# Optimization experiments

Hardware: AMD Instinct MI355X
Metric: run time of the kernel (lower is better)

## Reference

```python
import jax, jax.numpy as jnp
import numpy as np
from jax.scipy.linalg import solve_triangular

# Production config from MFAWrapper.from_path: 28x28 images, 50 components, 6 factors
B, DFT, K, L = 2048, 784, 50, 6
LOG2PI = float(np.log(2.0 * np.pi))


def setup_inputs() -> dict:
    key = jax.random.key(0)
    k1, k2, k3, k4, k5, k6 = jax.random.split(key, 6)
    X = jax.random.normal(k1, (B, DFT), dtype=jnp.float32)
    J = jax.random.randint(k2, (B, DFT), 0, 2).astype(jnp.int32)  # binary observation mask
    MU = jax.random.normal(k3, (K, DFT), dtype=jnp.float32) * 0.5
    A_fac = jax.random.normal(k4, (K, DFT, L), dtype=jnp.float32) * 0.1  # factor loadings
    log_D = jax.random.normal(k5, (K, DFT), dtype=jnp.float32) * 0.1 - 1.0  # log noise variances
    PI_logits = jax.random.normal(k6, (K,), dtype=jnp.float32)
    return {"X": X, "J": J, "MU": MU, "A_fac": A_fac, "log_D": log_D, "PI_logits": PI_logits}


def _mfa_conditional(X, J, MU, A_fac, log_D, PI_logits):
    """Batched MFA conditional reconstruction given observed features (mask J==1).

    The per-sample torch.nonzero selection is replaced by mask-weighted linear
    algebra: restricting to observed rows of diag(1/D) is identical to zeroing
    the unobserved entries of the weight, so all B samples are conditioned in
    one batched pass instead of a Python loop.
    """
    dtype = X.dtype
    l = A_fac.shape[-1]
    Jf = (J == 1).astype(dtype)                 # [B, Dft]
    inv_D = jnp.exp(-log_D)                     # [K, Dft]
    # masked residual per (sample, component): [B, K, Dft]
    md = (X[:, None, :] - MU[None, :, :]) * Jf[:, None, :]
    # latent posterior precision P = I + A_o^T D_o^{-1} A_o  -> [B, K, L, L]
    P = jnp.einsum('bd,kd,kdi,kdj->bkij', Jf, inv_D, A_fac, A_fac) + jnp.eye(l, dtype=dtype)
    # q = A_o^T D_o^{-1} (x_o - mu_o)  -> [B, K, L]
    q = jnp.einsum('bkd,kd,kdi->bki', md, inv_D, A_fac)
    # per-component log-likelihood of observed features via Woodbury / matrix det lemma
    Lc = jnp.linalg.cholesky(P)                                         # [B, K, L, L]
    y = solve_triangular(Lc, q[..., None], lower=True)[..., 0]          # [B, K, L]
    quad = jnp.einsum('bkd,kd->bk', md * md, inv_D) - jnp.sum(y * y, axis=-1)
    logdet = (2.0 * jnp.sum(jnp.log(jnp.diagonal(Lc, axis1=-2, axis2=-1)), axis=-1)
              + jnp.einsum('bd,kd->bk', Jf, log_D))
    n_obs = jnp.sum(Jf, axis=-1, keepdims=True)                         # [B, 1]
    log_lik = -0.5 * (quad + logdet + n_obs * LOG2PI)                   # [B, K]
    log_resp = jax.nn.log_softmax(PI_logits)[None, :] + log_lik
    c = jnp.argmax(log_resp, axis=-1)                                   # most responsible component, [B]
    # gather per-sample selected component and form the conditional Gaussian in factor form
    P_sel = jnp.take_along_axis(P, c[:, None, None, None], axis=1)[:, 0]  # [B, L, L]
    q_sel = jnp.take_along_axis(q, c[:, None, None], axis=1)[:, 0]        # [B, L]
    A_sel = A_fac[c]                                                      # [B, Dft, L]
    m_z = jnp.linalg.solve(P_sel, q_sel[..., None])[..., 0]               # posterior latent mean [B, L]
    cov_z = jnp.linalg.inv(P_sel)                                         # posterior latent cov [B, L, L]
    Lz = jnp.linalg.cholesky(cov_z)
    M = MU[c] + jnp.einsum('bdi,bi->bd', A_sel, m_z)                      # conditional mean over all features
    A_out = jnp.einsum('bdi,bij->bdj', A_sel, Lz)                         # loadings: cond cov = A_out A_out^T + diag(D_out)
    D_out = jnp.exp(log_D)[c]                                             # [B, Dft]
    Pw = jnp.ones((X.shape[0], 1), dtype)
    return Pw, M, A_out, D_out


def reference(X, J, MU, A_fac, log_D, PI_logits):
    return _mfa_conditional(X, J, MU, A_fac, log_D, PI_logits)
```

## Files before the change

kernel.cpp:

```cpp
#include <hip/hip_runtime.h>
#include <math.h>

#define B_N 2048
#define D_FT 784
#define K_N 50
#define L_N 6
#define LOG2PI_F 1.8378770664093453f

#define OUT_PW 0
#define OUT_M  (B_N)
#define OUT_A  (OUT_M + B_N*D_FT)
#define OUT_D  (OUT_A + B_N*D_FT*6)

#define WS_SCORES 0
#define WS_PQ     (WS_SCORES + K_N*B_N)
#define WS_XT     (WS_PQ + K_N*27*B_N)
#define WS_JBT    (WS_XT + D_FT*B_N)

#define IDX(i,j) ((i)*((i)+1)/2 + (j))

typedef float v2f __attribute__((ext_vector_type(2)));

#define PK_FMA(acc, a, b) asm("v_pk_fma_f32 %0, %1, %2, %0" : "+v"(acc) : "v"(a), "v"(b))
#define PK_MUL(dst, a, b) asm("v_pk_mul_f32 %0, %1, %2" : "=v"(dst) : "v"(a), "v"(b))
#define PK_ADD(dst, a, b) asm("v_pk_add_f32 %0, %1, %2" : "=v"(dst) : "v"(a), "v"(b))

__device__ __forceinline__ void chol6(const float* P, float* L, float* rd, float* sumlog) {
    float sl = 0.f;
    #pragma unroll
    for (int j = 0; j < 6; ++j) {
        float s = P[IDX(j,j)];
        #pragma unroll
        for (int m = 0; m < j; ++m) s -= L[IDX(j,m)] * L[IDX(j,m)];
        float d = sqrtf(s);
        L[IDX(j,j)] = d;
        float r = 1.0f / d;
        rd[j] = r;
        sl += logf(d);
        #pragma unroll
        for (int i = j + 1; i < 6; ++i) {
            float t = P[IDX(i,j)];
            #pragma unroll
            for (int m = 0; m < j; ++m) t -= L[IDX(i,m)] * L[IDX(j,m)];
            L[IDX(i,j)] = t * r;
        }
    }
    *sumlog = sl;
}

__global__ __launch_bounds__(1024) void k_prep(const float* __restrict__ X,
                                               const int* __restrict__ J,
                                               float4* __restrict__ Xt4,
                                               unsigned* __restrict__ JbT) {
    const int bid = blockIdx.x;
    const int tid = threadIdx.x;
    if (bid < 448) {
        __shared__ float4 tile[32][33];
        int tx = tid & 31, ty = tid >> 5;
        int d4b = (bid % 7) * 32;
        int bb  = (bid / 7) * 32;
        int d4 = d4b + tx;
        if (d4 < D_FT / 4)
            tile[ty][tx] = *(const float4*)&X[(size_t)(bb + ty) * D_FT + d4 * 4];
        __syncthreads();
        int d4o = d4b + ty;
        if (d4o < D_FT / 4)
            Xt4[(size_t)d4o * B_N + (bb + tx)] = tile[tx][ty];
    } else {
        int t = (bid - 448) * 1024 + tid;
        int b = t >> 5;
        int w = t & 31;
        if (w >= 25) return;
        int d0 = w * 32;
        int n = D_FT - d0; if (n > 32) n = 32;
        unsigned u = 0;
        for (int j = 0; j < n; ++j)
            u |= (J[(size_t)b * D_FT + d0 + j] != 0 ? 1u : 0u) << j;
        JbT[(size_t)w * B_N + b] = u;
    }
}

#define ACC_PAIR(pi, dd, x0, x1) do { \
    const v2f a0 = sld[(size_t)(pi) * 10 + 0]; \
    const v2f a1 = sld[(size_t)(pi) * 10 + 1]; \
    const v2f a2 = sld[(size_t)(pi) * 10 + 2]; \
    const v2f a3 = sld[(size_t)(pi) * 10 + 3]; \
    const v2f a4 = sld[(size_t)(pi) * 10 + 4]; \
    const v2f a5 = sld[(size_t)(pi) * 10 + 5]; \
    const v2f sa2  = sld[(size_t)(pi) * 10 + 6]; \
    const v2f nmu2 = sld[(size_t)(pi) * 10 + 7]; \
    const v2f l2   = sld[(size_t)(pi) * 10 + 8]; \
    v2f m2; m2.x = (float)((mw >> (dd)) & 1u); m2.y = (float)((mw >> ((dd)+1)) & 1u); \
    v2f x2; x2.x = (x0); x2.y = (x1); \
    v2f xm2; PK_ADD(xm2, x2, nmu2); \
    v2f w2;  PK_MUL(w2, m2, sa2); \
    v2f z2;  PK_MUL(z2, w2, xm2); \
    v2f u0, u1, u2v, u3, u4, u5; \
    PK_MUL(u0, m2, a0); PK_MUL(u1, m2, a1); PK_MUL(u2v, m2, a2); \
    PK_MUL(u3, m2, a3); PK_MUL(u4, m2, a4); PK_MUL(u5, m2, a5); \
    PK_FMA(jld2, m2, l2); \
    PK_FMA(Pm2[0],  u0, a0); \
    PK_FMA(Pm2[1],  u1, a0); PK_FMA(Pm2[2],  u1, a1); \
    PK_FMA(Pm2[3],  u2v, a0); PK_FMA(Pm2[4],  u2v, a1); PK_FMA(Pm2[5],  u2v, a2); \
    PK_FMA(Pm2[6],  u3, a0); PK_FMA(Pm2[7],  u3, a1); PK_FMA(Pm2[8],  u3, a2); PK_FMA(Pm2[9],  u3, a3); \
    PK_FMA(Pm2[10], u4, a0); PK_FMA(Pm2[11], u4, a1); PK_FMA(Pm2[12], u4, a2); PK_FMA(Pm2[13], u4, a3); PK_FMA(Pm2[14], u4, a4); \
    PK_FMA(Pm2[15], u5, a0); PK_FMA(Pm2[16], u5, a1); PK_FMA(Pm2[17], u5, a2); PK_FMA(Pm2[18], u5, a3); PK_FMA(Pm2[19], u5, a4); PK_FMA(Pm2[20], u5, a5); \
    PK_FMA(qv2[0], z2, a0); PK_FMA(qv2[1], z2, a1); PK_FMA(qv2[2], z2, a2); \
    PK_FMA(qv2[3], z2, a3); PK_FMA(qv2[4], z2, a4); PK_FMA(qv2[5], z2, a5); \
    PK_FMA(quad2, z2, z2); \
} while (0)

__global__ __launch_bounds__(256, 3) void k_accum(
        const float4* __restrict__ Xt4, const unsigned* __restrict__ JbT,
        const float* __restrict__ A, const float* __restrict__ MU,
        const float* __restrict__ logD, const float* __restrict__ PI,
        float* __restrict__ scores, float* __restrict__ Pq) {
    __shared__ v2f sld[200 * 10];
    float* smem = (float*)sld;
    float4* smf4 = (float4*)sld;
    const int k   = blockIdx.x >> 5;
    const int tid = threadIdx.x;
    const int s   = tid & 63;
    const int h   = tid >> 6;
    const int b   = (blockIdx.x & 31) * 64 + s;

    v2f Pm2[21], qv2[6], quad2, jld2;
    #pragma unroll
    for (int t = 0; t < 21; ++t) { Pm2[t].x = 0.f; Pm2[t].y = 0.f; }
    #pragma unroll
    for (int t = 0; t < 6; ++t) { qv2[t].x = 0.f; qv2[t].y = 0.f; }
    quad2.x = 0.f; quad2.y = 0.f;
    jld2.x = 0.f; jld2.y = 0.f;
    int nob = 0;

    for (int c = 0; c < 2; ++c) {
        const int dbase = c ? 384 : 0;
        const int npair = c ? 200 : 192;
        __syncthreads();
        for (int p = tid; p < npair; p += 256) {
            const int d0 = dbase + 2 * p;
            const float* ar0 = A + ((size_t)k * D_FT + d0) * 6;
            const float* ar1 = ar0 + 6;
            float ld0 = logD[(size_t)k * D_FT + d0];
            float ld1 = logD[(size_t)k * D_FT + d0 + 1];
            float sa0 = expf(-0.5f * ld0);
            float sa1 = expf(-0.5f * ld1);
            float4 f0, f1, f2, f3, f4;
            f0.x = sa0 * ar0[0]; f0.y = sa1 * ar1[0]; f0.z = sa0 * ar0[1]; f0.w = sa1 * ar1[1];
            f1.x = sa0 * ar0[2]; f1.y = sa1 * ar1[2]; f1.z = sa0 * ar0[3]; f1.w = sa1 * ar1[3];
            f2.x = sa0 * ar0[4]; f2.y = sa1 * ar1[4]; f2.z = sa0 * ar0[5]; f2.w = sa1 * ar1[5];
            f3.x = sa0; f3.y = sa1;
            f3.z = -MU[(size_t)k * D_FT + d0];
            f3.w = -MU[(size_t)k * D_FT + d0 + 1];
            f4.x = ld0; f4.y = ld1; f4.z = 0.f; f4.w = 0.f;
            smf4[(size_t)p * 5 + 0] = f0;
            smf4[(size_t)p * 5 + 1] = f1;
            smf4[(size_t)p * 5 + 2] = f2;
            smf4[(size_t)p * 5 + 3] = f3;
            smf4[(size_t)p * 5 + 4] = f4;
        }
        __syncthreads();

        const int wb = (c ? 12 : 0) + 3 * h;
        for (int w = wb; w < wb + 3; ++w) {
            const unsigned mw = JbT[(size_t)w * B_N + b];
            nob += __popc(mw);
            const int plb = w * 16 - (dbase >> 1);
            const float4* xp = Xt4 + (size_t)(w * 8) * B_N + b;
            #pragma unroll 2
            for (int g = 0; g < 8; ++g) {
                float4 xv = xp[(size_t)g * B_N];
                ACC_PAIR(plb + 2 * g,     g * 4,     xv.x, xv.y);
                ACC_PAIR(plb + 2 * g + 1, g * 4 + 2, xv.z, xv.w);
            }
        }
        if (c == 1 && h == 3) {
            const unsigned mw = JbT[(size_t)24 * B_N + b];
            nob += __popc(mw);
            const int plb = 24 * 16 - 192;
            const float4* xp = Xt4 + (size_t)(24 * 8) * B_N + b;
            #pragma unroll
            for (int g = 0; g < 4; ++g) {
                float4 xv = xp[(size_t)g * B_N];
                ACC_PAIR(plb + 2 * g,     g * 4,     xv.x, xv.y);
                ACC_PAIR(plb + 2 * g + 1, g * 4 + 2, xv.z, xv.w);
            }
        }
    }

    float Pm[21], qv[6], quad, jld;
    #pragma unroll
    for (int t = 0; t < 21; ++t) Pm[t] = Pm2[t].x + Pm2[t].y;
    #pragma unroll
    for (int t = 0; t < 6; ++t) qv[t] = qv2[t].x + qv2[t].y;
    quad = quad2.x + quad2.y;
    jld  = jld2.x + jld2.y;

    __syncthreads();
    float* red = smem;
    #define SLAB_WR do { float* o = &red[s * 33]; \
        _Pragma("unroll") for (int t = 0; t < 21; ++t) o[t] = Pm[t]; \
        _Pragma("unroll") for (int t = 0; t < 6; ++t) o[21 + t] = qv[t]; \
        o[27] = quad; o[28] = (float)nob; o[29] = jld; } while (0)
    #define SLAB_ADD do { const float* o = &red[s * 33]; \
        _Pragma("unroll") for (int t = 0; t < 21; ++t) Pm[t] += o[t]; \
        _Pragma("unroll") for (int t = 0; t < 6; ++t) qv[t] += o[21 + t]; \
        quad += o[27]; nob += (int)o[28]; jld += o[29]; } while (0)

    if (h == 1) SLAB_WR;
    __syncthreads();
    if (h == 0) SLAB_ADD;
    __syncthreads();
    if (h == 3) SLAB_WR;
    __syncthreads();
    if (h == 2) SLAB_ADD;
    __syncthreads();
    if (h == 2) SLAB_WR;
    __syncthreads();
    if (h == 0) {
        SLAB_ADD;
        float nobs = (float)nob;

        Pm[0] += 1.f; Pm[2] += 1.f; Pm[5] += 1.f; Pm[9] += 1.f; Pm[14] += 1.f; Pm[20] += 1.f;

        float Lm[21], rd[6], sumlog;
        chol6(Pm, Lm, rd, &sumlog);
        float y[6];
        #pragma unroll
        for (int j = 0; j < 6; ++j) {
            float sv = qv[j];
            #pragma unroll
            for (int m = 0; m < j; ++m) sv -= Lm[IDX(j,m)] * y[m];
            y[j] = sv * rd[j];
        }
        float yy = 0.f;
        #pragma unroll
        for (int j = 0; j < 6; ++j) yy += y[j] * y[j];
        float logdet = 2.f * sumlog + jld;
        float ll = -0.5f * ((quad - yy) + logdet + nobs * LOG2PI_F);
        float score = ll + PI[k];

        scores[(size_t)k * B_N + b] = score;
        float* pq = Pq + (size_t)k * 27 * B_N + b;
        #pragma unroll
        for (int t = 0; t < 21; ++t) pq[(size_t)t * B_N] = Pm[t];
        #pragma unroll
        for (int t = 0; t < 6; ++t) pq[(size_t)(21 + t) * B_N] = qv[t];
    }
}

__global__ __launch_bounds__(256) void k_outsel(
        const float* __restrict__ scores, const float* __restrict__ Pq,
        const float* __restrict__ A, const float* __restrict__ MU,
        const float* __restrict__ logD, float* __restrict__ out) {
    __shared__ float smz[6];
    __shared__ float sLz[21];
    __shared__ int sc;
    const int b = blockIdx.x;
    const int tid = threadIdx.x;

    if (tid < 64) {
        float best = scores[b];
        int bc = 0;
        for (int kk = 1; kk < K_N; ++kk) {
            float sv = scores[(size_t)kk * B_N + b];
            if (sv > best) { best = sv; bc = kk; }
        }

        float Pm[21], qv[6];
        const float* pq = Pq + (size_t)bc * 27 * B_N + b;
        #pragma unroll
        for (int t = 0; t < 21; ++t) Pm[t] = pq[(size_t)t * B_N];
        #pragma unroll
        for (int t = 0; t < 6; ++t) qv[t] = pq[(size_t)(21 + t) * B_N];

        float Lm[21], rd[6], dummy;
        chol6(Pm, Lm, rd, &dummy);

        float y[6];
        #pragma unroll
        for (int j = 0; j < 6; ++j) {
            float sv = qv[j];
            #pragma unroll
            for (int m = 0; m < j; ++m) sv -= Lm[IDX(j,m)] * y[m];
            y[j] = sv * rd[j];
        }
        float mz[6];
        #pragma unroll
        for (int ii = 5; ii >= 0; --ii) {
            float sv = y[ii];
            #pragma unroll
            for (int j = ii + 1; j < 6; ++j) sv -= Lm[IDX(j,ii)] * mz[j];
            mz[ii] = sv * rd[ii];
        }
        float Li[21];
        #pragma unroll
        for (int j = 0; j < 6; ++j) {
            Li[IDX(j,j)] = rd[j];
            #pragma unroll
            for (int i = j + 1; i < 6; ++i) {
                float sv = 0.f;
                #pragma unroll
                for (int m = j; m < i; ++m) sv += Lm[IDX(i,m)] * Li[IDX(m,j)];
                Li[IDX(i,j)] = -sv * rd[i];
            }
        }
        float cov[21];
        #pragma unroll
        for (int i = 0; i < 6; ++i) {
            #pragma unroll
            for (int j = 0; j <= i; ++j) {
                float sv = 0.f;
                #pragma unroll
                for (int m = i; m < 6; ++m) sv += Li[IDX(m,i)] * Li[IDX(m,j)];
                cov[IDX(i,j)] = sv;
            }
        }
        float Lz[21], rd2[6];
        chol6(cov, Lz, rd2, &dummy);

        if (tid == 0) {
            sc = bc;
            out[OUT_PW + b] = 1.0f;
            #pragma unroll
            for (int t = 0; t < 6; ++t) smz[t] = mz[t];
            #pragma unroll
            for (int t = 0; t < 21; ++t) sLz[t] = Lz[t];
        }
    }
    __syncthreads();
    const int c = sc;

    for (int d = tid; d < D_FT; d += 256) {
        const float* ar = A + ((size_t)c * D_FT + d) * 6;
        float a[6];
        #pragma unroll
        for (int i = 0; i < 6; ++i) a[i] = ar[i];
        float mu = MU[(size_t)c * D_FT + d];
        float ld = logD[(size_t)c * D_FT + d];
        float m = mu;
        #pragma unroll
        for (int i = 0; i < 6; ++i) m += a[i] * smz[i];
        out[OUT_M + (size_t)b * D_FT + d] = m;
        out[OUT_D + (size_t)b * D_FT + d] = expf(ld);
        float* ao = out + OUT_A + ((size_t)b * D_FT + d) * 6;
        #pragma unroll
        for (int j = 0; j < 6; ++j) {
            float sv = 0.f;
            #pragma unroll
            for (int i = j; i < 6; ++i) sv += a[i] * sLz[IDX(i,j)];
            ao[j] = sv;
        }
    }
}

extern "C" void kernel_launch(void* const* d_in, const int* in_sizes, int n_in,
                              void* d_out, int out_size, void* d_ws, size_t ws_size,
                              hipStream_t stream) {
    (void)in_sizes; (void)n_in; (void)out_size; (void)ws_size;
    const float* X    = (const float*)d_in[0];
    const int*   J    = (const int*)d_in[1];
    const float* MU   = (const float*)d_in[2];
    const float* A    = (const float*)d_in[3];
    const float* logD = (const float*)d_in[4];
    const float* PI   = (const float*)d_in[5];
    float* out = (float*)d_out;
    float* ws  = (float*)d_ws;

    float*    scores = ws + WS_SCORES;
    float*    Pq     = ws + WS_PQ;
    float4*   Xt4    = (float4*)(ws + WS_XT);
    unsigned* JbT    = (unsigned*)(ws + WS_JBT);

    k_prep<<<512, 1024, 0, stream>>>(X, J, Xt4, JbT);

    k_accum<<<32 * K_N, 256, 0, stream>>>(Xt4, JbT, A, MU, logD, PI, scores, Pq);

    k_outsel<<<B_N, 256, 0, stream>>>(scores, Pq, A, MU, logD, out);
}
```

Before: 116.1 us.

## Precompute per-component weight records and read them via scalar constant loads

Adds a prep stage that writes per-component records holding A, exp(-logD) and -MU, plus a separate logD array, to the workspace. The accumulation kernel no longer stages these into LDS with block barriers. It reads them through address_space(4) pointers so the compiler can issue wave-uniform scalar loads, and the packed v_pk_fma math becomes scalar fmaf. This removes the LDS fill and its syncs and lowers LDS use, but drops the packed-FP32 throughput and needs an extra workspace region.

```diff
diff --git a/kernel.cpp b/kernel.cpp
--- a/kernel.cpp
+++ b/kernel.cpp
@@ -16,14 +16,12 @@
 #define WS_PQ     (WS_SCORES + K_N*B_N)
 #define WS_XT     (WS_PQ + K_N*27*B_N)
 #define WS_JBT    (WS_XT + D_FT*B_N)
+#define WS_WREC   (WS_JBT + 25*B_N)
+#define WS_WLD    (WS_WREC + K_N*D_FT*8)
 
 #define IDX(i,j) ((i)*((i)+1)/2 + (j))
 
-typedef float v2f __attribute__((ext_vector_type(2)));
-
-#define PK_FMA(acc, a, b) asm("v_pk_fma_f32 %0, %1, %2, %0" : "+v"(acc) : "v"(a), "v"(b))
-#define PK_MUL(dst, a, b) asm("v_pk_mul_f32 %0, %1, %2" : "=v"(dst) : "v"(a), "v"(b))
-#define PK_ADD(dst, a, b) asm("v_pk_add_f32 %0, %1, %2" : "=v"(dst) : "v"(a), "v"(b))
+#define CAS const __attribute__((address_space(4)))
 
 __device__ __forceinline__ void chol6(const float* P, float* L, float* rd, float* sumlog) {
     float sl = 0.f;
@@ -50,8 +48,13 @@
 
 __global__ __launch_bounds__(1024) void k_prep(const float* __restrict__ X,
                                                const int* __restrict__ J,
+                                               const float* __restrict__ A,
+                                               const float* __restrict__ MU,
+                                               const float* __restrict__ logD,
                                                float4* __restrict__ Xt4,
-                                               unsigned* __restrict__ JbT) {
+                                               unsigned* __restrict__ JbT,
+                                               float* __restrict__ Wrec,
+                                               float* __restrict__ Wld) {
     const int bid = blockIdx.x;
     const int tid = threadIdx.x;
     if (bid < 448) {
@@ -66,7 +69,7 @@
         int d4o = d4b + ty;
         if (d4o < D_FT / 4)
             Xt4[(size_t)d4o * B_N + (bb + tx)] = tile[tx][ty];
-    } else {
+    } else if (bid < 512) {
         int t = (bid - 448) * 1024 + tid;
         int b = t >> 5;
         int w = t & 31;
@@ -77,127 +80,101 @@
         for (int j = 0; j < n; ++j)
             u |= (J[(size_t)b * D_FT + d0 + j] != 0 ? 1u : 0u) << j;
         JbT[(size_t)w * B_N + b] = u;
-    }
-}
-
-#define ACC_PAIR(pi, dd, x0, x1) do { \
-    const v2f a0 = sld[(size_t)(pi) * 10 + 0]; \
-    const v2f a1 = sld[(size_t)(pi) * 10 + 1]; \
-    const v2f a2 = sld[(size_t)(pi) * 10 + 2]; \
-    const v2f a3 = sld[(size_t)(pi) * 10 + 3]; \
-    const v2f a4 = sld[(size_t)(pi) * 10 + 4]; \
-    const v2f a5 = sld[(size_t)(pi) * 10 + 5]; \
-    const v2f sa2  = sld[(size_t)(pi) * 10 + 6]; \
-    const v2f nmu2 = sld[(size_t)(pi) * 10 + 7]; \
-    const v2f l2   = sld[(size_t)(pi) * 10 + 8]; \
-    v2f m2; m2.x = (float)((mw >> (dd)) & 1u); m2.y = (float)((mw >> ((dd)+1)) & 1u); \
-    v2f x2; x2.x = (x0); x2.y = (x1); \
-    v2f xm2; PK_ADD(xm2, x2, nmu2); \
-    v2f w2;  PK_MUL(w2, m2, sa2); \
-    v2f z2;  PK_MUL(z2, w2, xm2); \
-    v2f u0, u1, u2v, u3, u4, u5; \
-    PK_MUL(u0, m2, a0); PK_MUL(u1, m2, a1); PK_MUL(u2v, m2, a2); \
-    PK_MUL(u3, m2, a3); PK_MUL(u4, m2, a4); PK_MUL(u5, m2, a5); \
-    PK_FMA(jld2, m2, l2); \
-    PK_FMA(Pm2[0],  u0, a0); \
-    PK_FMA(Pm2[1],  u1, a0); PK_FMA(Pm2[2],  u1, a1); \
-    PK_FMA(Pm2[3],  u2v, a0); PK_FMA(Pm2[4],  u2v, a1); PK_FMA(Pm2[5],  u2v, a2); \
-    PK_FMA(Pm2[6],  u3, a0); PK_FMA(Pm2[7],  u3, a1); PK_FMA(Pm2[8],  u3, a2); PK_FMA(Pm2[9],  u3, a3); \
-    PK_FMA(Pm2[10], u4, a0); PK_FMA(Pm2[11], u4, a1); PK_FMA(Pm2[12], u4, a2); PK_FMA(Pm2[13], u4, a3); PK_FMA(Pm2[14], u4, a4); \
-    PK_FMA(Pm2[15], u5, a0); PK_FMA(Pm2[16], u5, a1); PK_FMA(Pm2[17], u5, a2); PK_FMA(Pm2[18], u5, a3); PK_FMA(Pm2[19], u5, a4); PK_FMA(Pm2[20], u5, a5); \
-    PK_FMA(qv2[0], z2, a0); PK_FMA(qv2[1], z2, a1); PK_FMA(qv2[2], z2, a2); \
-    PK_FMA(qv2[3], z2, a3); PK_FMA(qv2[4], z2, a4); PK_FMA(qv2[5], z2, a5); \
-    PK_FMA(quad2, z2, z2); \
+    } else {
+        const int k = bid - 512;
+        for (int d = tid; d < D_FT; d += 1024) {
+            const float* ar = A + ((size_t)k * D_FT + d) * 6;
+            float ld = logD[(size_t)k * D_FT + d];
+            float4 r0, r1;
+            r0.x = ar[0]; r0.y = ar[1]; r0.z = ar[2]; r0.w = ar[3];
+            r1.x = ar[4]; r1.y = ar[5];
+            r1.z = expf(-ld);
+            r1.w = -MU[(size_t)k * D_FT + d];
+            float4* wr = (float4*)(Wrec + ((size_t)k * D_FT + d) * 8);
+            wr[0] = r0; wr[1] = r1;
+            Wld[(size_t)k * D_FT + d] = ld;
+        }
+    }
+}
+
+#define ACC_D(di, dd, xval) do { \
+    const size_t ro = (size_t)(di) * 8; \
+    const float a0 = Wr[ro + 0], a1 = Wr[ro + 1], a2 = Wr[ro + 2]; \
+    const float a3 = Wr[ro + 3], a4 = Wr[ro + 4], a5 = Wr[ro + 5]; \
+    const float iD = Wr[ro + 6], nmu = Wr[ro + 7]; \
+    const float ldv = Wl[(di)]; \
+    const float m = (float)((mw >> (dd)) & 1u); \
+    const float wgt = m * iD; \
+    const float z = (xval) + nmu; \
+    const float t = wgt * z; \
+    quad = fmaf(t, z, quad); \
+    jld  = fmaf(m, ldv, jld); \
+    const float u0 = wgt*a0, u1 = wgt*a1, u2 = wgt*a2; \
+    const float u3 = wgt*a3, u4 = wgt*a4, u5 = wgt*a5; \
+    Pm[0]  = fmaf(u0, a0, Pm[0]); \
+    Pm[1]  = fmaf(u1, a0, Pm[1]);  Pm[2]  = fmaf(u1, a1, Pm[2]); \
+    Pm[3]  = fmaf(u2, a0, Pm[3]);  Pm[4]  = fmaf(u2, a1, Pm[4]);  Pm[5]  = fmaf(u2, a2, Pm[5]); \
+    Pm[6]  = fmaf(u3, a0, Pm[6]);  Pm[7]  = fmaf(u3, a1, Pm[7]);  Pm[8]  = fmaf(u3, a2, Pm[8]);  Pm[9]  = fmaf(u3, a3, Pm[9]); \
+    Pm[10] = fmaf(u4, a0, Pm[10]); Pm[11] = fmaf(u4, a1, Pm[11]); Pm[12] = fmaf(u4, a2, Pm[12]); Pm[13] = fmaf(u4, a3, Pm[13]); Pm[14] = fmaf(u4, a4, Pm[14]); \
+    Pm[15] = fmaf(u5, a0, Pm[15]); Pm[16] = fmaf(u5, a1, Pm[16]); Pm[17] = fmaf(u5, a2, Pm[17]); Pm[18] = fmaf(u5, a3, Pm[18]); Pm[19] = fmaf(u5, a4, Pm[19]); Pm[20] = fmaf(u5, a5, Pm[20]); \
+    qv[0] = fmaf(t, a0, qv[0]); qv[1] = fmaf(t, a1, qv[1]); qv[2] = fmaf(t, a2, qv[2]); \
+    qv[3] = fmaf(t, a3, qv[3]); qv[4] = fmaf(t, a4, qv[4]); qv[5] = fmaf(t, a5, qv[5]); \
 } while (0)
 
 __global__ __launch_bounds__(256, 3) void k_accum(
         const float4* __restrict__ Xt4, const unsigned* __restrict__ JbT,
-        const float* __restrict__ A, const float* __restrict__ MU,
-        const float* __restrict__ logD, const float* __restrict__ PI,
+        const float* __restrict__ WrecG, const float* __restrict__ WldG,
+        const float* __restrict__ PI,
         float* __restrict__ scores, float* __restrict__ Pq) {
-    __shared__ v2f sld[200 * 10];
-    float* smem = (float*)sld;
-    float4* smf4 = (float4*)sld;
+    __shared__ float red[64 * 33];
     const int k   = blockIdx.x >> 5;
     const int tid = threadIdx.x;
     const int s   = tid & 63;
     const int h   = tid >> 6;
     const int b   = (blockIdx.x & 31) * 64 + s;
 
-    v2f Pm2[21], qv2[6], quad2, jld2;
+    CAS float* Wr = (CAS float*)(uintptr_t)(WrecG + (size_t)k * D_FT * 8);
+    CAS float* Wl = (CAS float*)(uintptr_t)(WldG + (size_t)k * D_FT);
+
+    float Pm[21], qv[6];
     #pragma unroll
-    for (int t = 0; t < 21; ++t) { Pm2[t].x = 0.f; Pm2[t].y = 0.f; }
+    for (int t = 0; t < 21; ++t) Pm[t] = 0.f;
     #pragma unroll
-    for (int t = 0; t < 6; ++t) { qv2[t].x = 0.f; qv2[t].y = 0.f; }
-    quad2.x = 0.f; quad2.y = 0.f;
-    jld2.x = 0.f; jld2.y = 0.f;
+    for (int t = 0; t < 6; ++t) qv[t] = 0.f;
+    float quad = 0.f, jld = 0.f;
     int nob = 0;
 
-    for (int c = 0; c < 2; ++c) {
-        const int dbase = c ? 384 : 0;
-        const int npair = c ? 200 : 192;
-        __syncthreads();
-        for (int p = tid; p < npair; p += 256) {
-            const int d0 = dbase + 2 * p;
-            const float* ar0 = A + ((size_t)k * D_FT + d0) * 6;
-            const float* ar1 = ar0 + 6;
-            float ld0 = logD[(size_t)k * D_FT + d0];
-            float ld1 = logD[(size_t)k * D_FT + d0 + 1];
-            float sa0 = expf(-0.5f * ld0);
-            float sa1 = expf(-0.5f * ld1);
-            float4 f0, f1, f2, f3, f4;
-            f0.x = sa0 * ar0[0]; f0.y = sa1 * ar1[0]; f0.z = sa0 * ar0[1]; f0.w = sa1 * ar1[1];
-            f1.x = sa0 * ar0[2]; f1.y = sa1 * ar1[2]; f1.z = sa0 * ar0[3]; f1.w = sa1 * ar1[3];
-            f2.x = sa0 * ar0[4]; f2.y = sa1 * ar1[4]; f2.z = sa0 * ar0[5]; f2.w = sa1 * ar1[5];
-            f3.x = sa0; f3.y = sa1;
-            f3.z = -MU[(size_t)k * D_FT + d0];
-            f3.w = -MU[(size_t)k * D_FT + d0 + 1];
-            f4.x = ld0; f4.y = ld1; f4.z = 0.f; f4.w = 0.f;
-            smf4[(size_t)p * 5 + 0] = f0;
-            smf4[(size_t)p * 5 + 1] = f1;
-            smf4[(size_t)p * 5 + 2] = f2;
-            smf4[(size_t)p * 5 + 3] = f3;
-            smf4[(size_t)p * 5 + 4] = f4;
-        }
-        __syncthreads();
-
-        const int wb = (c ? 12 : 0) + 3 * h;
-        for (int w = wb; w < wb + 3; ++w) {
-            const unsigned mw = JbT[(size_t)w * B_N + b];
-            nob += __popc(mw);
-            const int plb = w * 16 - (dbase >> 1);
-            const float4* xp = Xt4 + (size_t)(w * 8) * B_N + b;
-            #pragma unroll 2
-            for (int g = 0; g < 8; ++g) {
-                float4 xv = xp[(size_t)g * B_N];
-                ACC_PAIR(plb + 2 * g,     g * 4,     xv.x, xv.y);
-                ACC_PAIR(plb + 2 * g + 1, g * 4 + 2, xv.z, xv.w);
-            }
-        }
-        if (c == 1 && h == 3) {
-            const unsigned mw = JbT[(size_t)24 * B_N + b];
-            nob += __popc(mw);
-            const int plb = 24 * 16 - 192;
-            const float4* xp = Xt4 + (size_t)(24 * 8) * B_N + b;
-            #pragma unroll
-            for (int g = 0; g < 4; ++g) {
-                float4 xv = xp[(size_t)g * B_N];
-                ACC_PAIR(plb + 2 * g,     g * 4,     xv.x, xv.y);
-                ACC_PAIR(plb + 2 * g + 1, g * 4 + 2, xv.z, xv.w);
-            }
-        }
-    }
-
-    float Pm[21], qv[6], quad, jld;
-    #pragma unroll
-    for (int t = 0; t < 21; ++t) Pm[t] = Pm2[t].x + Pm2[t].y;
-    #pragma unroll
-    for (int t = 0; t < 6; ++t) qv[t] = qv2[t].x + qv2[t].y;
-    quad = quad2.x + quad2.y;
-    jld  = jld2.x + jld2.y;
-
-    __syncthreads();
-    float* red = smem;
+    const int w0 = 6 * h;
+    const int w1 = (h == 3) ? 24 : (6 * h + 6);
+    for (int w = w0; w < w1; ++w) {
+        const unsigned mw = JbT[(size_t)w * B_N + b];
+        nob += __popc(mw);
+        const int dwb = w * 32;
+        const float4* xp = Xt4 + (size_t)(w * 8) * B_N + b;
+        #pragma unroll 4
+        for (int g = 0; g < 8; ++g) {
+            float4 xv = xp[(size_t)g * B_N];
+            ACC_D(dwb + 4 * g + 0, 4 * g + 0, xv.x);
+            ACC_D(dwb + 4 * g + 1, 4 * g + 1, xv.y);
+            ACC_D(dwb + 4 * g + 2, 4 * g + 2, xv.z);
+            ACC_D(dwb + 4 * g + 3, 4 * g + 3, xv.w);
+        }
+    }
+    if (h == 3) {
+        const unsigned mw = JbT[(size_t)24 * B_N + b];
+        nob += __popc(mw);
+        const int dwb = 768;
+        const float4* xp = Xt4 + (size_t)(24 * 8) * B_N + b;
+        #pragma unroll
+        for (int g = 0; g < 4; ++g) {
+            float4 xv = xp[(size_t)g * B_N];
+            ACC_D(dwb + 4 * g + 0, 4 * g + 0, xv.x);
+            ACC_D(dwb + 4 * g + 1, 4 * g + 1, xv.y);
+            ACC_D(dwb + 4 * g + 2, 4 * g + 2, xv.z);
+            ACC_D(dwb + 4 * g + 3, 4 * g + 3, xv.w);
+        }
+    }
+
     #define SLAB_WR do { float* o = &red[s * 33]; \
         _Pragma("unroll") for (int t = 0; t < 21; ++t) o[t] = Pm[t]; \
         _Pragma("unroll") for (int t = 0; t < 6; ++t) o[21 + t] = qv[t]; \
@@ -371,10 +348,12 @@
     float*    Pq     = ws + WS_PQ;
     float4*   Xt4    = (float4*)(ws + WS_XT);
     unsigned* JbT    = (unsigned*)(ws + WS_JBT);
-
-    k_prep<<<512, 1024, 0, stream>>>(X, J, Xt4, JbT);
-
-    k_accum<<<32 * K_N, 256, 0, stream>>>(Xt4, JbT, A, MU, logD, PI, scores, Pq);
+    float*    Wrec   = ws + WS_WREC;
+    float*    Wld    = ws + WS_WLD;
+
+    k_prep<<<562, 1024, 0, stream>>>(X, J, A, MU, logD, Xt4, JbT, Wrec, Wld);
+
+    k_accum<<<32 * K_N, 256, 0, stream>>>(Xt4, JbT, Wrec, Wld, PI, scores, Pq);
 
     k_outsel<<<B_N, 256, 0, stream>>>(scores, Pq, A, MU, logD, out);
 }
```

Result: slower. 160.9 us (+38.6%).
